# Optimization experiments

Hardware: AMD Instinct MI355X
Metric: run time of the kernel (lower is better)

The kernel has to match this reference:

```python
import jax, jax.numpy as jnp
import numpy as np

N = 8192
F_IN, HID, LAT = 256, 128, 32


def setup_inputs() -> dict:
    key = jax.random.key(0)
    k1, k2, k3, k4 = jax.random.split(key, 4)
    X = jax.random.normal(k1, (N, F_IN), dtype=jnp.float32)
    # Dense normalized-adjacency stand-in (original converts dense A_tilde to COO each call)
    A_tilde = jax.random.uniform(k2, (N, N), dtype=jnp.float32) / N
    # Xavier-uniform init like torch's init.xavier_uniform_ on Linear weights
    lim1 = float(np.sqrt(6.0 / (F_IN + HID)))
    lim2 = float(np.sqrt(6.0 / (HID + LAT)))
    W1 = jax.random.uniform(k3, (F_IN, HID), dtype=jnp.float32, minval=-lim1, maxval=lim1)
    W2 = jax.random.uniform(k4, (HID, LAT), dtype=jnp.float32, minval=-lim2, maxval=lim2)
    return {"X": X, "A_tilde": A_tilde, "W1": W1, "W2": W2}


def reference(X, A_tilde, W1, W2):
    # GCN layer 1: A_tilde @ (X W1), then ReLU
    h = jax.nn.relu(A_tilde @ (X @ W1))          # [N, HID]
    # GCN layer 2 (no activation)
    Z = A_tilde @ (h @ W2)                        # [N, LAT]
    # Inner-product decoder
    A_hat = jax.nn.sigmoid(Z @ Z.T)               # [N, N]
    return A_hat
```

## Files before the change

### kernel.cpp

```cpp
#include <hip/hip_runtime.h>
#include <hip/hip_bf16.h>

#define N_ 8192
#define F_ 256
#define H_ 128
#define L_ 32

typedef __attribute__((ext_vector_type(8))) short bf16x8;
typedef __attribute__((ext_vector_type(4))) float f32x4;
typedef __attribute__((ext_vector_type(4))) short bf16x4;

__device__ __forceinline__ unsigned f2bf_u(float x) {
    unsigned u = __builtin_bit_cast(unsigned, x);
    return (u + 0x7fffu + ((u >> 16) & 1u)) >> 16;
}
__device__ __forceinline__ short f2bf(float x) { return (short)f2bf_u(x); }

__device__ __forceinline__ bf16x8 cvt8(float4 a, float4 b) {
    bf16x8 v;
    v[0] = f2bf(a.x); v[1] = f2bf(a.y); v[2] = f2bf(a.z); v[3] = f2bf(a.w);
    v[4] = f2bf(b.x); v[5] = f2bf(b.y); v[6] = f2bf(b.z); v[7] = f2bf(b.w);
    return v;
}

__global__ __launch_bounds__(256) void k1_xw1(const float* __restrict__ X,
                                              const float* __restrict__ W1,
                                              short* __restrict__ XW1T) {
    __shared__ short w1t[H_ * (F_ + 8)];
    const int tid = threadIdx.x;
    for (int idx = tid; idx < F_ * H_; idx += 256) {
        int k = idx >> 7, n = idx & 127;
        w1t[n * (F_ + 8) + k] = f2bf(W1[idx]);
    }
    __syncthreads();
    const int wv = tid >> 6, l = tid & 63;
    const int lm = l & 15, q = l >> 4;
    const int i0 = blockIdx.x * 64 + wv * 16;
    const float* xrow = X + (size_t)(i0 + lm) * F_;
    f32x4 acc[8];
#pragma unroll
    for (int j = 0; j < 8; ++j) acc[j] = (f32x4){0.f, 0.f, 0.f, 0.f};
#pragma unroll
    for (int k0 = 0; k0 < F_; k0 += 32) {
        float4 a0 = *(const float4*)(xrow + k0 + q * 8);
        float4 a1 = *(const float4*)(xrow + k0 + q * 8 + 4);
        bf16x8 af = cvt8(a0, a1);
#pragma unroll
        for (int j = 0; j < 8; ++j) {
            bf16x8 bf = *(const bf16x8*)&w1t[(j * 16 + lm) * (F_ + 8) + k0 + q * 8];
            acc[j] = __builtin_amdgcn_mfma_f32_16x16x32_bf16(af, bf, acc[j], 0, 0, 0);
        }
    }
#pragma unroll
    for (int j = 0; j < 8; ++j) {
        bf16x4 o;
        o[0] = f2bf(acc[j][0]); o[1] = f2bf(acc[j][1]);
        o[2] = f2bf(acc[j][2]); o[3] = f2bf(acc[j][3]);
        *(bf16x4*)(XW1T + (size_t)(j * 16 + lm) * N_ + i0 + q * 4) = o;
    }
}

__global__ __launch_bounds__(512) void k2_h_zp(const float* __restrict__ A,
                                               const short* __restrict__ XW1T,
                                               const float* __restrict__ W2,
                                               short* __restrict__ ZPT) {
    __shared__ float lacc[4][32][H_ + 4];
    __shared__ short hl[32 * (H_ + 8)];
    __shared__ short w2t[L_ * (H_ + 8)];
    const int tid = threadIdx.x;
    for (int idx = tid; idx < H_ * L_; idx += 512) {
        int k = idx >> 5, j = idx & 31;
        w2t[j * (H_ + 8) + k] = f2bf(W2[idx]);
    }
    const int wv = tid >> 6, l = tid & 63;
    const int lm = l & 15, q = l >> 4;
    const int s = wv & 1, kq = wv >> 1;
    const int i0 = blockIdx.x * 32;
    const float* arow = A + (size_t)(i0 + s * 16 + lm) * N_;
    f32x4 acc[8];
#pragma unroll
    for (int j = 0; j < 8; ++j) acc[j] = (f32x4){0.f, 0.f, 0.f, 0.f};
    const int kbeg = kq * (N_ / 4), kend = kbeg + N_ / 4;
#pragma unroll 4
    for (int k0 = kbeg; k0 < kend; k0 += 32) {
        float4 a0 = *(const float4*)(arow + k0 + q * 8);
        float4 a1 = *(const float4*)(arow + k0 + q * 8 + 4);
        bf16x8 af = cvt8(a0, a1);
#pragma unroll
        for (int j = 0; j < 8; ++j) {
            bf16x8 bf = *(const bf16x8*)(XW1T + (size_t)(j * 16 + lm) * N_ + k0 + q * 8);
            acc[j] = __builtin_amdgcn_mfma_f32_16x16x32_bf16(af, bf, acc[j], 0, 0, 0);
        }
    }
#pragma unroll
    for (int j = 0; j < 8; ++j)
#pragma unroll
        for (int r = 0; r < 4; ++r)
            lacc[kq][s * 16 + q * 4 + r][j * 16 + lm] = acc[j][r];
    __syncthreads();
    for (int e = tid; e < 32 * H_; e += 512) {
        int rr = e >> 7, c = e & 127;
        float v = (lacc[0][rr][c] + lacc[1][rr][c]) + (lacc[2][rr][c] + lacc[3][rr][c]);
        hl[rr * (H_ + 8) + c] = f2bf(v > 0.f ? v : 0.f);
    }
    __syncthreads();
    if (wv < 4) {
        const int ti = wv & 1, tj = wv >> 1;
        f32x4 a2 = (f32x4){0.f, 0.f, 0.f, 0.f};
#pragma unroll
        for (int k0 = 0; k0 < H_; k0 += 32) {
            bf16x8 af = *(const bf16x8*)&hl[(ti * 16 + lm) * (H_ + 8) + k0 + q * 8];
            bf16x8 bf = *(const bf16x8*)&w2t[(tj * 16 + lm) * (H_ + 8) + k0 + q * 8];
            a2 = __builtin_amdgcn_mfma_f32_16x16x32_bf16(af, bf, a2, 0, 0, 0);
        }
        bf16x4 o;
        o[0] = f2bf(a2[0]); o[1] = f2bf(a2[1]); o[2] = f2bf(a2[2]); o[3] = f2bf(a2[3]);
        *(bf16x4*)(ZPT + (size_t)(tj * 16 + lm) * N_ + i0 + ti * 16 + q * 4) = o;
    }
}

__global__ __launch_bounds__(512) void k3_z(const float* __restrict__ A,
                                            const short* __restrict__ ZPT,
                                            short* __restrict__ Z) {
    __shared__ float lacc[4][32][L_ + 4];
    const int tid = threadIdx.x;
    const int wv = tid >> 6, l = tid & 63;
    const int lm = l & 15, q = l >> 4;
    const int s = wv & 1, kq = wv >> 1;
    const int i0 = blockIdx.x * 32;
    const float* arow = A + (size_t)(i0 + s * 16 + lm) * N_;
    f32x4 acc[2];
    acc[0] = (f32x4){0.f, 0.f, 0.f, 0.f};
    acc[1] = (f32x4){0.f, 0.f, 0.f, 0.f};
    const int kbeg = kq * (N_ / 4), kend = kbeg + N_ / 4;
#pragma unroll 4
    for (int k0 = kbeg; k0 < kend; k0 += 32) {
        float4 a0 = *(const float4*)(arow + k0 + q * 8);
        float4 a1 = *(const float4*)(arow + k0 + q * 8 + 4);
        bf16x8 af = cvt8(a0, a1);
#pragma unroll
        for (int j = 0; j < 2; ++j) {
            bf16x8 bf = *(const bf16x8*)(ZPT + (size_t)(j * 16 + lm) * N_ + k0 + q * 8);
            acc[j] = __builtin_amdgcn_mfma_f32_16x16x32_bf16(af, bf, acc[j], 0, 0, 0);
        }
    }
#pragma unroll
    for (int j = 0; j < 2; ++j)
#pragma unroll
        for (int r = 0; r < 4; ++r)
            lacc[kq][s * 16 + q * 4 + r][j * 16 + lm] = acc[j][r];
    __syncthreads();
    {
        int e = tid * 2;
        int rr = e >> 5, c = e & 31;
        float v0 = (lacc[0][rr][c] + lacc[1][rr][c]) + (lacc[2][rr][c] + lacc[3][rr][c]);
        float v1 = (lacc[0][rr][c + 1] + lacc[1][rr][c + 1]) + (lacc[2][rr][c + 1] + lacc[3][rr][c + 1]);
        unsigned pk = f2bf_u(v0) | (f2bf_u(v1) << 16);
        *(unsigned*)(Z + (size_t)(i0 + rr) * L_ + c) = pk;
    }
}

__global__ __launch_bounds__(256) void k4_dec(const short* __restrict__ Z,
                                              float* __restrict__ out) {
    const int tid = threadIdx.x;
    const int wv = tid >> 6, l = tid & 63;
    const int lm = l & 15, q = l >> 4;
    const int bj = blockIdx.x & 63, bi = blockIdx.x >> 6;
    const int i0 = bi * 128, j0 = bj * 128;
    bf16x8 af[2];
#pragma unroll
    for (int t = 0; t < 2; ++t)
        af[t] = *(const bf16x8*)(Z + (size_t)(i0 + wv * 32 + t * 16 + lm) * L_ + q * 8);
#pragma unroll
    for (int tj = 0; tj < 8; ++tj) {
        bf16x8 bf = *(const bf16x8*)(Z + (size_t)(j0 + tj * 16 + lm) * L_ + q * 8);
#pragma unroll
        for (int t = 0; t < 2; ++t) {
            f32x4 c = __builtin_amdgcn_mfma_f32_16x16x32_bf16(
                af[t], bf, (f32x4){0.f, 0.f, 0.f, 0.f}, 0, 0, 0);
            const int gi = i0 + wv * 32 + t * 16 + q * 4;
            float* op = out + (size_t)gi * N_ + j0 + tj * 16 + lm;
#pragma unroll
            for (int r = 0; r < 4; ++r) {
                float e = __expf(-c[r]);
                op[(size_t)r * N_] = __fdividef(1.f, 1.f + e);
            }
        }
    }
}

extern "C" void kernel_launch(void* const* d_in, const int* in_sizes, int n_in,
                              void* d_out, int out_size, void* d_ws, size_t ws_size,
                              hipStream_t stream) {
    const float* X  = (const float*)d_in[0];
    const float* A  = (const float*)d_in[1];
    const float* W1 = (const float*)d_in[2];
    const float* W2 = (const float*)d_in[3];
    float* out = (float*)d_out;

    short* XW1T = (short*)d_ws;
    short* ZPT  = XW1T + (size_t)H_ * N_;
    short* Z    = ZPT + (size_t)L_ * N_;

    k1_xw1<<<N_ / 64, 256, 0, stream>>>(X, W1, XW1T);
    k2_h_zp<<<N_ / 32, 512, 0, stream>>>(A, XW1T, W2, ZPT);
    k3_z<<<N_ / 32, 512, 0, stream>>>(A, ZPT, Z);
    k4_dec<<<(N_ / 128) * (N_ / 128), 256, 0, stream>>>(Z, out);
}
```

Measured before the change: 631.6 us.

## Stage A and B tiles through double-buffered LDS in GEMMs; stage decoder output

The two A-multiplication kernels now load A and the B operand cooperatively with coalesced wide loads into double-buffered shared-memory tiles, with register prefetch two stages ahead. This replaces per-lane strided global fragment loads, and the k2 split-K reduction through LDS is replaced by a column split. The decoder now writes sigmoid results to an LDS tile first and then stores full rows as float4, giving coalesced output writes. In exchange the kernels need more LDS and a barrier on every k-step, which can lower occupancy.

```diff
diff --git a/kernel.cpp b/kernel.cpp
--- a/kernel.cpp
+++ b/kernel.cpp
@@ -5,6 +5,7 @@
 #define F_ 256
 #define H_ 128
 #define L_ 32
+#define BK 64
 
 typedef __attribute__((ext_vector_type(8))) short bf16x8;
 typedef __attribute__((ext_vector_type(4))) float f32x4;
@@ -16,6 +17,11 @@
 }
 __device__ __forceinline__ short f2bf(float x) { return (short)f2bf_u(x); }
 
+__device__ __forceinline__ bf16x4 cvt4(float4 a) {
+    bf16x4 v;
+    v[0] = f2bf(a.x); v[1] = f2bf(a.y); v[2] = f2bf(a.z); v[3] = f2bf(a.w);
+    return v;
+}
 __device__ __forceinline__ bf16x8 cvt8(float4 a, float4 b) {
     bf16x8 v;
     v[0] = f2bf(a.x); v[1] = f2bf(a.y); v[2] = f2bf(a.z); v[3] = f2bf(a.w);
@@ -64,104 +70,162 @@
                                                const short* __restrict__ XW1T,
                                                const float* __restrict__ W2,
                                                short* __restrict__ ZPT) {
-    __shared__ float lacc[4][32][H_ + 4];
-    __shared__ short hl[32 * (H_ + 8)];
-    __shared__ short w2t[L_ * (H_ + 8)];
+    __shared__ short As[2][32][72];
+    __shared__ short Bs[2][128][72];
+    __shared__ short hl[32][136];
+    __shared__ short w2t[32][136];
     const int tid = threadIdx.x;
     for (int idx = tid; idx < H_ * L_; idx += 512) {
         int k = idx >> 5, j = idx & 31;
-        w2t[j * (H_ + 8) + k] = f2bf(W2[idx]);
-    }
-    const int wv = tid >> 6, l = tid & 63;
-    const int lm = l & 15, q = l >> 4;
-    const int s = wv & 1, kq = wv >> 1;
+        w2t[j][k] = f2bf(W2[idx]);
+    }
+    const int wv = tid >> 6, l = tid & 63, lm = l & 15, q = l >> 4;
+    const int rs = wv & 1, cs = wv >> 1;
     const int i0 = blockIdx.x * 32;
-    const float* arow = A + (size_t)(i0 + s * 16 + lm) * N_;
-    f32x4 acc[8];
-#pragma unroll
-    for (int j = 0; j < 8; ++j) acc[j] = (f32x4){0.f, 0.f, 0.f, 0.f};
-    const int kbeg = kq * (N_ / 4), kend = kbeg + N_ / 4;
-#pragma unroll 4
-    for (int k0 = kbeg; k0 < kend; k0 += 32) {
-        float4 a0 = *(const float4*)(arow + k0 + q * 8);
-        float4 a1 = *(const float4*)(arow + k0 + q * 8 + 4);
-        bf16x8 af = cvt8(a0, a1);
-#pragma unroll
-        for (int j = 0; j < 8; ++j) {
-            bf16x8 bf = *(const bf16x8*)(XW1T + (size_t)(j * 16 + lm) * N_ + k0 + q * 8);
-            acc[j] = __builtin_amdgcn_mfma_f32_16x16x32_bf16(af, bf, acc[j], 0, 0, 0);
-        }
-    }
-#pragma unroll
-    for (int j = 0; j < 8; ++j)
-#pragma unroll
-        for (int r = 0; r < 4; ++r)
-            lacc[kq][s * 16 + q * 4 + r][j * 16 + lm] = acc[j][r];
-    __syncthreads();
-    for (int e = tid; e < 32 * H_; e += 512) {
-        int rr = e >> 7, c = e & 127;
-        float v = (lacc[0][rr][c] + lacc[1][rr][c]) + (lacc[2][rr][c] + lacc[3][rr][c]);
-        hl[rr * (H_ + 8) + c] = f2bf(v > 0.f ? v : 0.f);
-    }
+    const int ar = tid >> 4, ac = (tid & 15) * 4;
+    const int br = tid >> 2, bc = (tid & 3) * 16;
+    const float* Arow = A + (size_t)(i0 + ar) * N_ + ac;
+    const short* Brow = XW1T + (size_t)br * N_ + bc;
+
+    float4 pa[2]; bf16x8 pb0[2], pb1[2];
+    pa[0]  = *(const float4*)(Arow);
+    pb0[0] = *(const bf16x8*)(Brow);
+    pb1[0] = *(const bf16x8*)(Brow + 8);
+    pa[1]  = *(const float4*)(Arow + BK);
+    pb0[1] = *(const bf16x8*)(Brow + BK);
+    pb1[1] = *(const bf16x8*)(Brow + BK + 8);
+    *(bf16x4*)&As[0][ar][ac] = cvt4(pa[0]);
+    *(bf16x8*)&Bs[0][br][bc] = pb0[0];
+    *(bf16x8*)&Bs[0][br][bc + 8] = pb1[0];
+    pa[0]  = *(const float4*)(Arow + 2 * BK);
+    pb0[0] = *(const bf16x8*)(Brow + 2 * BK);
+    pb1[0] = *(const bf16x8*)(Brow + 2 * BK + 8);
+    __syncthreads();
+
+    f32x4 acc[2];
+    acc[0] = (f32x4){0.f, 0.f, 0.f, 0.f};
+    acc[1] = (f32x4){0.f, 0.f, 0.f, 0.f};
+    const int NS = N_ / BK;
+#pragma unroll 2
+    for (int s = 0; s < NS; ++s) {
+        const int buf = s & 1;
+#pragma unroll
+        for (int kh = 0; kh < 2; ++kh) {
+            bf16x8 af = *(const bf16x8*)&As[buf][rs * 16 + lm][kh * 32 + q * 8];
+#pragma unroll
+            for (int jt = 0; jt < 2; ++jt) {
+                bf16x8 bf = *(const bf16x8*)&Bs[buf][cs * 32 + jt * 16 + lm][kh * 32 + q * 8];
+                acc[jt] = __builtin_amdgcn_mfma_f32_16x16x32_bf16(af, bf, acc[jt], 0, 0, 0);
+            }
+        }
+        if (s + 1 < NS) {
+            const int p = (s + 1) & 1;
+            *(bf16x4*)&As[p][ar][ac] = cvt4(pa[p]);
+            *(bf16x8*)&Bs[p][br][bc] = pb0[p];
+            *(bf16x8*)&Bs[p][br][bc + 8] = pb1[p];
+            if (s + 3 < NS) {
+                pa[p]  = *(const float4*)(Arow + (s + 3) * BK);
+                pb0[p] = *(const bf16x8*)(Brow + (s + 3) * BK);
+                pb1[p] = *(const bf16x8*)(Brow + (s + 3) * BK + 8);
+            }
+        }
+        __syncthreads();
+    }
+#pragma unroll
+    for (int jt = 0; jt < 2; ++jt)
+#pragma unroll
+        for (int r = 0; r < 4; ++r) {
+            float v = acc[jt][r];
+            hl[rs * 16 + q * 4 + r][cs * 32 + jt * 16 + lm] = f2bf(v > 0.f ? v : 0.f);
+        }
     __syncthreads();
     if (wv < 4) {
-        const int ti = wv & 1, tj = wv >> 1;
+        const int ti = wv & 1, tjw = wv >> 1;
         f32x4 a2 = (f32x4){0.f, 0.f, 0.f, 0.f};
 #pragma unroll
         for (int k0 = 0; k0 < H_; k0 += 32) {
-            bf16x8 af = *(const bf16x8*)&hl[(ti * 16 + lm) * (H_ + 8) + k0 + q * 8];
-            bf16x8 bf = *(const bf16x8*)&w2t[(tj * 16 + lm) * (H_ + 8) + k0 + q * 8];
+            bf16x8 af = *(const bf16x8*)&hl[ti * 16 + lm][k0 + q * 8];
+            bf16x8 bf = *(const bf16x8*)&w2t[tjw * 16 + lm][k0 + q * 8];
             a2 = __builtin_amdgcn_mfma_f32_16x16x32_bf16(af, bf, a2, 0, 0, 0);
         }
         bf16x4 o;
         o[0] = f2bf(a2[0]); o[1] = f2bf(a2[1]); o[2] = f2bf(a2[2]); o[3] = f2bf(a2[3]);
-        *(bf16x4*)(ZPT + (size_t)(tj * 16 + lm) * N_ + i0 + ti * 16 + q * 4) = o;
+        *(bf16x4*)(ZPT + (size_t)(tjw * 16 + lm) * N_ + i0 + ti * 16 + q * 4) = o;
     }
 }
 
 __global__ __launch_bounds__(512) void k3_z(const float* __restrict__ A,
                                             const short* __restrict__ ZPT,
                                             short* __restrict__ Z) {
-    __shared__ float lacc[4][32][L_ + 4];
-    const int tid = threadIdx.x;
-    const int wv = tid >> 6, l = tid & 63;
-    const int lm = l & 15, q = l >> 4;
-    const int s = wv & 1, kq = wv >> 1;
+    __shared__ short As[2][2][32][72];
+    __shared__ short Bs[2][2][32][72];
+    __shared__ float lacc[2][32][36];
+    const int tid = threadIdx.x;
+    const int wv = tid >> 6, l = tid & 63, lm = l & 15, q = l >> 4;
+    const int kq = wv >> 2, rs = (wv >> 1) & 1, cs = wv & 1;
     const int i0 = blockIdx.x * 32;
-    const float* arow = A + (size_t)(i0 + s * 16 + lm) * N_;
-    f32x4 acc[2];
-    acc[0] = (f32x4){0.f, 0.f, 0.f, 0.f};
-    acc[1] = (f32x4){0.f, 0.f, 0.f, 0.f};
-    const int kbeg = kq * (N_ / 4), kend = kbeg + N_ / 4;
-#pragma unroll 4
-    for (int k0 = kbeg; k0 < kend; k0 += 32) {
-        float4 a0 = *(const float4*)(arow + k0 + q * 8);
-        float4 a1 = *(const float4*)(arow + k0 + q * 8 + 4);
-        bf16x8 af = cvt8(a0, a1);
-#pragma unroll
-        for (int j = 0; j < 2; ++j) {
-            bf16x8 bf = *(const bf16x8*)(ZPT + (size_t)(j * 16 + lm) * N_ + k0 + q * 8);
-            acc[j] = __builtin_amdgcn_mfma_f32_16x16x32_bf16(af, bf, acc[j], 0, 0, 0);
-        }
-    }
-#pragma unroll
-    for (int j = 0; j < 2; ++j)
-#pragma unroll
-        for (int r = 0; r < 4; ++r)
-            lacc[kq][s * 16 + q * 4 + r][j * 16 + lm] = acc[j][r];
+    const int ar = (tid >> 4) & 31, ac = (tid & 15) * 4;
+    const int bkw = tid >> 8, br = (tid >> 3) & 31, bc = (tid & 7) * 8;
+    const float* Ar0 = A + (size_t)(i0 + ar) * N_ + ac;
+    const float* Ar1 = Ar0 + N_ / 2;
+    const short* Brow = ZPT + (size_t)br * N_ + bc + bkw * (N_ / 2);
+
+    float4 pa0[2], pa1[2]; bf16x8 pb[2];
+    pa0[0] = *(const float4*)(Ar0);
+    pa1[0] = *(const float4*)(Ar1);
+    pb[0]  = *(const bf16x8*)(Brow);
+    pa0[1] = *(const float4*)(Ar0 + BK);
+    pa1[1] = *(const float4*)(Ar1 + BK);
+    pb[1]  = *(const bf16x8*)(Brow + BK);
+    *(bf16x4*)&As[0][0][ar][ac] = cvt4(pa0[0]);
+    *(bf16x4*)&As[0][1][ar][ac] = cvt4(pa1[0]);
+    *(bf16x8*)&Bs[0][bkw][br][bc] = pb[0];
+    pa0[0] = *(const float4*)(Ar0 + 2 * BK);
+    pa1[0] = *(const float4*)(Ar1 + 2 * BK);
+    pb[0]  = *(const bf16x8*)(Brow + 2 * BK);
+    __syncthreads();
+
+    f32x4 acc = (f32x4){0.f, 0.f, 0.f, 0.f};
+    const int NS = (N_ / 2) / BK;
+#pragma unroll 2
+    for (int s = 0; s < NS; ++s) {
+        const int buf = s & 1;
+#pragma unroll
+        for (int kh = 0; kh < 2; ++kh) {
+            bf16x8 af = *(const bf16x8*)&As[buf][kq][rs * 16 + lm][kh * 32 + q * 8];
+            bf16x8 bf = *(const bf16x8*)&Bs[buf][kq][cs * 16 + lm][kh * 32 + q * 8];
+            acc = __builtin_amdgcn_mfma_f32_16x16x32_bf16(af, bf, acc, 0, 0, 0);
+        }
+        if (s + 1 < NS) {
+            const int p = (s + 1) & 1;
+            *(bf16x4*)&As[p][0][ar][ac] = cvt4(pa0[p]);
+            *(bf16x4*)&As[p][1][ar][ac] = cvt4(pa1[p]);
+            *(bf16x8*)&Bs[p][bkw][br][bc] = pb[p];
+            if (s + 3 < NS) {
+                pa0[p] = *(const float4*)(Ar0 + (s + 3) * BK);
+                pa1[p] = *(const float4*)(Ar1 + (s + 3) * BK);
+                pb[p]  = *(const bf16x8*)(Brow + (s + 3) * BK);
+            }
+        }
+        __syncthreads();
+    }
+#pragma unroll
+    for (int r = 0; r < 4; ++r)
+        lacc[kq][rs * 16 + q * 4 + r][cs * 16 + lm] = acc[r];
     __syncthreads();
     {
         int e = tid * 2;
-        int rr = e >> 5, c = e & 31;
-        float v0 = (lacc[0][rr][c] + lacc[1][rr][c]) + (lacc[2][rr][c] + lacc[3][rr][c]);
-        float v1 = (lacc[0][rr][c + 1] + lacc[1][rr][c + 1]) + (lacc[2][rr][c + 1] + lacc[3][rr][c + 1]);
+        int row = e >> 5, c = e & 31;
+        float v0 = lacc[0][row][c] + lacc[1][row][c];
+        float v1 = lacc[0][row][c + 1] + lacc[1][row][c + 1];
         unsigned pk = f2bf_u(v0) | (f2bf_u(v1) << 16);
-        *(unsigned*)(Z + (size_t)(i0 + rr) * L_ + c) = pk;
+        *(unsigned*)(Z + (size_t)(i0 + row) * L_ + c) = pk;
     }
 }
 
 __global__ __launch_bounds__(256) void k4_dec(const short* __restrict__ Z,
                                               float* __restrict__ out) {
+    __shared__ float os[128][132];
     const int tid = threadIdx.x;
     const int wv = tid >> 6, l = tid & 63;
     const int lm = l & 15, q = l >> 4;
@@ -173,19 +237,22 @@
         af[t] = *(const bf16x8*)(Z + (size_t)(i0 + wv * 32 + t * 16 + lm) * L_ + q * 8);
 #pragma unroll
     for (int tj = 0; tj < 8; ++tj) {
-        bf16x8 bf = *(const bf16x8*)(Z + (size_t)(j0 + tj * 16 + lm) * L_ + q * 8);
+        bf16x8 bfv = *(const bf16x8*)(Z + (size_t)(j0 + tj * 16 + lm) * L_ + q * 8);
 #pragma unroll
         for (int t = 0; t < 2; ++t) {
             f32x4 c = __builtin_amdgcn_mfma_f32_16x16x32_bf16(
-                af[t], bf, (f32x4){0.f, 0.f, 0.f, 0.f}, 0, 0, 0);
-            const int gi = i0 + wv * 32 + t * 16 + q * 4;
-            float* op = out + (size_t)gi * N_ + j0 + tj * 16 + lm;
+                af[t], bfv, (f32x4){0.f, 0.f, 0.f, 0.f}, 0, 0, 0);
 #pragma unroll
             for (int r = 0; r < 4; ++r) {
                 float e = __expf(-c[r]);
-                op[(size_t)r * N_] = __fdividef(1.f, 1.f + e);
-            }
-        }
+                os[wv * 32 + t * 16 + q * 4 + r][tj * 16 + lm] = __fdividef(1.f, 1.f + e);
+            }
+        }
+    }
+    __syncthreads();
+    for (int idx = tid; idx < 128 * 32; idx += 256) {
+        int row = idx >> 5, c4 = idx & 31;
+        *(float4*)(out + (size_t)(i0 + row) * N_ + j0 + c4 * 4) = *(const float4*)&os[row][c4 * 4];
     }
 }
 
```

Result: faster. 565.4 us (-10.5%).

## Pre-convert adjacency to bf16, pipeline GEMM loads, stage decoder output through LDS

Applied to the files above, without the earlier changes.

Adds a pass that converts the fp32 adjacency matrix to bf16 in workspace, so both big A-multiplies read half the bytes and skip per-iteration conversion. The k2/k3 kernels are restructured to 16-row blocks of 256 threads with a software double-buffered register prefetch of A and B fragments. The decoder now writes sigmoid results into shared memory and emits coalesced float4 row stores. The cost is an extra full read of fp32 A plus a bf16 write and reread, and the workspace must be large enough for an N×N bf16 copy.

```diff
diff --git a/kernel.cpp b/kernel.cpp
--- a/kernel.cpp
+++ b/kernel.cpp
@@ -23,6 +23,14 @@
     return v;
 }
 
+__global__ __launch_bounds__(256) void k0_cvt(const float* __restrict__ A,
+                                              short* __restrict__ Ab) {
+    size_t g = ((size_t)blockIdx.x * 256 + threadIdx.x) * 8;
+    float4 a = *(const float4*)(A + g);
+    float4 b = *(const float4*)(A + g + 4);
+    *(bf16x8*)(Ab + g) = cvt8(a, b);
+}
+
 __global__ __launch_bounds__(256) void k1_xw1(const float* __restrict__ X,
                                               const float* __restrict__ W1,
                                               short* __restrict__ XW1T) {
@@ -60,95 +68,117 @@
     }
 }
 
-__global__ __launch_bounds__(512) void k2_h_zp(const float* __restrict__ A,
+__global__ __launch_bounds__(256) void k2_h_zp(const short* __restrict__ Ab,
                                                const short* __restrict__ XW1T,
                                                const float* __restrict__ W2,
                                                short* __restrict__ ZPT) {
-    __shared__ float lacc[4][32][H_ + 4];
-    __shared__ short hl[32 * (H_ + 8)];
-    __shared__ short w2t[L_ * (H_ + 8)];
-    const int tid = threadIdx.x;
-    for (int idx = tid; idx < H_ * L_; idx += 512) {
+    __shared__ float lacc[4][16][132];
+    __shared__ short hl[16][136];
+    __shared__ short w2t[32][136];
+    const int tid = threadIdx.x;
+    for (int idx = tid; idx < H_ * L_; idx += 256) {
         int k = idx >> 5, j = idx & 31;
-        w2t[j * (H_ + 8) + k] = f2bf(W2[idx]);
-    }
-    const int wv = tid >> 6, l = tid & 63;
-    const int lm = l & 15, q = l >> 4;
-    const int s = wv & 1, kq = wv >> 1;
-    const int i0 = blockIdx.x * 32;
-    const float* arow = A + (size_t)(i0 + s * 16 + lm) * N_;
+        w2t[j][k] = f2bf(W2[idx]);
+    }
+    const int wv = tid >> 6, l = tid & 63, lm = l & 15, q = l >> 4;
+    const int i0 = blockIdx.x * 16;
+    const int kbeg = wv * (N_ / 4);
+    const short* Arow = Ab + (size_t)(i0 + lm) * N_ + kbeg + q * 8;
+    const short* Bp[8];
+#pragma unroll
+    for (int jt = 0; jt < 8; ++jt)
+        Bp[jt] = XW1T + (size_t)(jt * 16 + lm) * N_ + kbeg + q * 8;
+
+    bf16x8 pa[2], pb[2][8];
+#pragma unroll
+    for (int t = 0; t < 2; ++t) {
+        pa[t] = *(const bf16x8*)(Arow + t * 32);
+#pragma unroll
+        for (int jt = 0; jt < 8; ++jt) pb[t][jt] = *(const bf16x8*)(Bp[jt] + t * 32);
+    }
     f32x4 acc[8];
 #pragma unroll
     for (int j = 0; j < 8; ++j) acc[j] = (f32x4){0.f, 0.f, 0.f, 0.f};
-    const int kbeg = kq * (N_ / 4), kend = kbeg + N_ / 4;
-#pragma unroll 4
-    for (int k0 = kbeg; k0 < kend; k0 += 32) {
-        float4 a0 = *(const float4*)(arow + k0 + q * 8);
-        float4 a1 = *(const float4*)(arow + k0 + q * 8 + 4);
-        bf16x8 af = cvt8(a0, a1);
-#pragma unroll
-        for (int j = 0; j < 8; ++j) {
-            bf16x8 bf = *(const bf16x8*)(XW1T + (size_t)(j * 16 + lm) * N_ + k0 + q * 8);
-            acc[j] = __builtin_amdgcn_mfma_f32_16x16x32_bf16(af, bf, acc[j], 0, 0, 0);
-        }
-    }
-#pragma unroll
-    for (int j = 0; j < 8; ++j)
+
+    const int NS = (N_ / 4) / 32;
+#pragma unroll 2
+    for (int s = 0; s < NS; ++s) {
+        const int p = s & 1;
+        bf16x8 af = pa[p];
+#pragma unroll
+        for (int jt = 0; jt < 8; ++jt)
+            acc[jt] = __builtin_amdgcn_mfma_f32_16x16x32_bf16(af, pb[p][jt], acc[jt], 0, 0, 0);
+        if (s + 2 < NS) {
+            pa[p] = *(const bf16x8*)(Arow + (s + 2) * 32);
+#pragma unroll
+            for (int jt = 0; jt < 8; ++jt)
+                pb[p][jt] = *(const bf16x8*)(Bp[jt] + (s + 2) * 32);
+        }
+    }
+#pragma unroll
+    for (int jt = 0; jt < 8; ++jt)
 #pragma unroll
         for (int r = 0; r < 4; ++r)
-            lacc[kq][s * 16 + q * 4 + r][j * 16 + lm] = acc[j][r];
-    __syncthreads();
-    for (int e = tid; e < 32 * H_; e += 512) {
+            lacc[wv][q * 4 + r][jt * 16 + lm] = acc[jt][r];
+    __syncthreads();
+    for (int e = tid; e < 16 * H_; e += 256) {
         int rr = e >> 7, c = e & 127;
         float v = (lacc[0][rr][c] + lacc[1][rr][c]) + (lacc[2][rr][c] + lacc[3][rr][c]);
-        hl[rr * (H_ + 8) + c] = f2bf(v > 0.f ? v : 0.f);
-    }
-    __syncthreads();
-    if (wv < 4) {
-        const int ti = wv & 1, tj = wv >> 1;
+        hl[rr][c] = f2bf(v > 0.f ? v : 0.f);
+    }
+    __syncthreads();
+    if (wv < 2) {
         f32x4 a2 = (f32x4){0.f, 0.f, 0.f, 0.f};
 #pragma unroll
         for (int k0 = 0; k0 < H_; k0 += 32) {
-            bf16x8 af = *(const bf16x8*)&hl[(ti * 16 + lm) * (H_ + 8) + k0 + q * 8];
-            bf16x8 bf = *(const bf16x8*)&w2t[(tj * 16 + lm) * (H_ + 8) + k0 + q * 8];
-            a2 = __builtin_amdgcn_mfma_f32_16x16x32_bf16(af, bf, a2, 0, 0, 0);
+            bf16x8 af2 = *(const bf16x8*)&hl[lm][k0 + q * 8];
+            bf16x8 bf2 = *(const bf16x8*)&w2t[wv * 16 + lm][k0 + q * 8];
+            a2 = __builtin_amdgcn_mfma_f32_16x16x32_bf16(af2, bf2, a2, 0, 0, 0);
         }
         bf16x4 o;
         o[0] = f2bf(a2[0]); o[1] = f2bf(a2[1]); o[2] = f2bf(a2[2]); o[3] = f2bf(a2[3]);
-        *(bf16x4*)(ZPT + (size_t)(tj * 16 + lm) * N_ + i0 + ti * 16 + q * 4) = o;
-    }
-}
-
-__global__ __launch_bounds__(512) void k3_z(const float* __restrict__ A,
+        *(bf16x4*)(ZPT + (size_t)(wv * 16 + lm) * N_ + i0 + q * 4) = o;
+    }
+}
+
+__global__ __launch_bounds__(256) void k3_z(const short* __restrict__ Ab,
                                             const short* __restrict__ ZPT,
                                             short* __restrict__ Z) {
-    __shared__ float lacc[4][32][L_ + 4];
-    const int tid = threadIdx.x;
-    const int wv = tid >> 6, l = tid & 63;
-    const int lm = l & 15, q = l >> 4;
-    const int s = wv & 1, kq = wv >> 1;
-    const int i0 = blockIdx.x * 32;
-    const float* arow = A + (size_t)(i0 + s * 16 + lm) * N_;
-    f32x4 acc[2];
-    acc[0] = (f32x4){0.f, 0.f, 0.f, 0.f};
-    acc[1] = (f32x4){0.f, 0.f, 0.f, 0.f};
-    const int kbeg = kq * (N_ / 4), kend = kbeg + N_ / 4;
-#pragma unroll 4
-    for (int k0 = kbeg; k0 < kend; k0 += 32) {
-        float4 a0 = *(const float4*)(arow + k0 + q * 8);
-        float4 a1 = *(const float4*)(arow + k0 + q * 8 + 4);
-        bf16x8 af = cvt8(a0, a1);
-#pragma unroll
-        for (int j = 0; j < 2; ++j) {
-            bf16x8 bf = *(const bf16x8*)(ZPT + (size_t)(j * 16 + lm) * N_ + k0 + q * 8);
-            acc[j] = __builtin_amdgcn_mfma_f32_16x16x32_bf16(af, bf, acc[j], 0, 0, 0);
-        }
-    }
-#pragma unroll
-    for (int j = 0; j < 2; ++j)
-#pragma unroll
-        for (int r = 0; r < 4; ++r)
-            lacc[kq][s * 16 + q * 4 + r][j * 16 + lm] = acc[j][r];
+    __shared__ float lacc[4][16][36];
+    const int tid = threadIdx.x;
+    const int wv = tid >> 6, l = tid & 63, lm = l & 15, q = l >> 4;
+    const int i0 = blockIdx.x * 16;
+    const int kbeg = wv * (N_ / 4);
+    const short* Arow = Ab + (size_t)(i0 + lm) * N_ + kbeg + q * 8;
+    const short* Bp0 = ZPT + (size_t)lm * N_ + kbeg + q * 8;
+    const short* Bp1 = Bp0 + (size_t)16 * N_;
+
+    bf16x8 pa[2], pb0[2], pb1[2];
+#pragma unroll
+    for (int t = 0; t < 2; ++t) {
+        pa[t]  = *(const bf16x8*)(Arow + t * 32);
+        pb0[t] = *(const bf16x8*)(Bp0 + t * 32);
+        pb1[t] = *(const bf16x8*)(Bp1 + t * 32);
+    }
+    f32x4 acc0 = (f32x4){0.f, 0.f, 0.f, 0.f};
+    f32x4 acc1 = (f32x4){0.f, 0.f, 0.f, 0.f};
+    const int NS = (N_ / 4) / 32;
+#pragma unroll 2
+    for (int s = 0; s < NS; ++s) {
+        const int p = s & 1;
+        acc0 = __builtin_amdgcn_mfma_f32_16x16x32_bf16(pa[p], pb0[p], acc0, 0, 0, 0);
+        acc1 = __builtin_amdgcn_mfma_f32_16x16x32_bf16(pa[p], pb1[p], acc1, 0, 0, 0);
+        if (s + 2 < NS) {
+            pa[p]  = *(const bf16x8*)(Arow + (s + 2) * 32);
+            pb0[p] = *(const bf16x8*)(Bp0 + (s + 2) * 32);
+            pb1[p] = *(const bf16x8*)(Bp1 + (s + 2) * 32);
+        }
+    }
+#pragma unroll
+    for (int r = 0; r < 4; ++r) {
+        lacc[wv][q * 4 + r][lm]      = acc0[r];
+        lacc[wv][q * 4 + r][16 + lm] = acc1[r];
+    }
     __syncthreads();
     {
         int e = tid * 2;
@@ -162,6 +192,7 @@
 
 __global__ __launch_bounds__(256) void k4_dec(const short* __restrict__ Z,
                                               float* __restrict__ out) {
+    __shared__ float os[128][132];
     const int tid = threadIdx.x;
     const int wv = tid >> 6, l = tid & 63;
     const int lm = l & 15, q = l >> 4;
@@ -173,19 +204,22 @@
         af[t] = *(const bf16x8*)(Z + (size_t)(i0 + wv * 32 + t * 16 + lm) * L_ + q * 8);
 #pragma unroll
     for (int tj = 0; tj < 8; ++tj) {
-        bf16x8 bf = *(const bf16x8*)(Z + (size_t)(j0 + tj * 16 + lm) * L_ + q * 8);
+        bf16x8 bfv = *(const bf16x8*)(Z + (size_t)(j0 + tj * 16 + lm) * L_ + q * 8);
 #pragma unroll
         for (int t = 0; t < 2; ++t) {
             f32x4 c = __builtin_amdgcn_mfma_f32_16x16x32_bf16(
-                af[t], bf, (f32x4){0.f, 0.f, 0.f, 0.f}, 0, 0, 0);
-            const int gi = i0 + wv * 32 + t * 16 + q * 4;
-            float* op = out + (size_t)gi * N_ + j0 + tj * 16 + lm;
+                af[t], bfv, (f32x4){0.f, 0.f, 0.f, 0.f}, 0, 0, 0);
 #pragma unroll
             for (int r = 0; r < 4; ++r) {
                 float e = __expf(-c[r]);
-                op[(size_t)r * N_] = __fdividef(1.f, 1.f + e);
+                os[wv * 32 + t * 16 + q * 4 + r][tj * 16 + lm] = __fdividef(1.f, 1.f + e);
             }
         }
+    }
+    __syncthreads();
+    for (int idx = tid; idx < 128 * 32; idx += 256) {
+        int row = idx >> 5, c4 = idx & 31;
+        *(float4*)(out + (size_t)(i0 + row) * N_ + j0 + c4 * 4) = *(const float4*)&os[row][c4 * 4];
     }
 }
 
@@ -201,9 +235,11 @@
     short* XW1T = (short*)d_ws;
     short* ZPT  = XW1T + (size_t)H_ * N_;
     short* Z    = ZPT + (size_t)L_ * N_;
+    short* Ab   = Z + (size_t)N_ * L_;
 
     k1_xw1<<<N_ / 64, 256, 0, stream>>>(X, W1, XW1T);
-    k2_h_zp<<<N_ / 32, 512, 0, stream>>>(A, XW1T, W2, ZPT);
-    k3_z<<<N_ / 32, 512, 0, stream>>>(A, ZPT, Z);
+    k0_cvt<<<(N_ * N_) / (256 * 8), 256, 0, stream>>>(A, Ab);
+    k2_h_zp<<<N_ / 16, 256, 0, stream>>>(Ab, XW1T, W2, ZPT);
+    k3_z<<<N_ / 16, 256, 0, stream>>>(Ab, ZPT, Z);
     k4_dec<<<(N_ / 128) * (N_ / 128), 256, 0, stream>>>(Z, out);
 }
```

Result: slower. 672.9 us (+6.5%).
